# Kernel optimization log

Measured on AMD Instinct MI355X. Metric: run time of the kernel, lower is better.

Reference implementation:

```python
import jax, jax.numpy as jnp
import numpy as np

B, T, C, H = 4, 2048, 1024, 16
D = C // H  # head dim = 64


def setup_inputs() -> dict:
    key = jax.random.key(0)
    ks = jax.random.split(key, 8)
    s = 1.0 / np.sqrt(C)
    return {
        "x": jax.random.normal(ks[0], (B, T, C), jnp.float32),
        "mask": jax.random.randint(ks[1], (B, T), 0, 2, jnp.int32),
        "Wq": jax.random.normal(ks[2], (C, C), jnp.float32) * s,
        "bq": jnp.zeros((C,), jnp.float32),
        "Wk": jax.random.normal(ks[3], (C, C), jnp.float32) * s,
        "bk": jnp.zeros((C,), jnp.float32),
        "Wv": jax.random.normal(ks[4], (C, C), jnp.float32) * s,
        "bv": jnp.zeros((C,), jnp.float32),
    }


def reference(x, mask, Wq, bq, Wk, bk, Wv, bv):
    # QKV projections (nn.Linear: x @ W.T + b); W stored here as [out,in] -> use W.T
    q = x @ Wq.T + bq
    k = x @ Wk.T + bk
    v = x @ Wv.T + bv
    # split heads: [B,T,C] -> [B,H,T,D]
    q = q.reshape(B, T, H, D).transpose(0, 2, 1, 3)
    k = k.reshape(B, T, H, D).transpose(0, 2, 1, 3)
    v = v.reshape(B, T, H, D).transpose(0, 2, 1, 3)
    # scaled dot-product attention scores [B,H,T,T]
    attn = jnp.einsum("bhqd,bhkd->bhqk", q, k) / jnp.sqrt(jnp.float32(D))
    # additive mask over key positions: attn - inf*(1-mask), expressed stably
    big_neg = jnp.float32(-1e30)
    attn = jnp.where(mask[:, None, None, :] > 0, attn, big_neg)
    attn = jax.nn.softmax(attn, axis=-1)
    # dropout p=0 -> identity
    y = jnp.einsum("bhqk,bhkd->bhqd", attn, v)
    # merge heads: [B,H,T,D] -> [B,T,C]
    return y.transpose(0, 2, 1, 3).reshape(B, T, C)
```

## Files before the change

kernel.cpp:

```cpp
#include <hip/hip_runtime.h>
#include <stdint.h>

#define BB 4
#define TT 2048
#define CC 1024
#define HH 16
#define DD 64
#define MM (BB * TT)

typedef unsigned short u16;
typedef unsigned int   u32;
typedef __attribute__((ext_vector_type(8))) short short8;
typedef _Float16 half8  __attribute__((ext_vector_type(8)));
typedef __fp16   fp16x2 __attribute__((ext_vector_type(2)));
typedef __attribute__((ext_vector_type(4))) float f32x4;
typedef __attribute__((ext_vector_type(4))) unsigned short u16x4;
typedef __attribute__((ext_vector_type(4))) unsigned int u32x4;

#if __has_builtin(__builtin_amdgcn_exp2f)
#define EXP2(x) __builtin_amdgcn_exp2f(x)
#else
#define EXP2(x) __expf(0.69314718055994531f * (x))
#endif

__device__ inline u16 f2bf(float f) {
    union { float f; unsigned u; } v; v.f = f;
    unsigned r = 0x7fffu + ((v.u >> 16) & 1u);
    return (u16)((v.u + r) >> 16);
}
__device__ inline u16 f2h(float f) {
    union { _Float16 h; u16 u; } c; c.h = (_Float16)f; return c.u;
}
__device__ inline u32 pkh(float a, float b) {
    union { fp16x2 h; u32 u; } c;
    c.h = __builtin_amdgcn_cvt_pkrtz(a, b);
    return c.u;
}
__device__ inline u32 pkmask(int a, int b) {
    return ((u32)(-a) & 0xFFFFu) | ((u32)(-b) << 16);
}

#define NX (MM * CC / 4)
#define NW (CC * CC / 4)
__global__ void cvt_all(const float* __restrict__ x,  const float* __restrict__ Wq,
                        const float* __restrict__ Wk, const float* __restrict__ Wv,
                        u16* __restrict__ xb, u16* __restrict__ Wb) {
    int i = blockIdx.x * blockDim.x + threadIdx.x;
    const float* src; u16* dst; int j;
    if (i < NX)               { src = x;  dst = xb;                       j = i; }
    else if (i < NX + NW)     { src = Wq; dst = Wb;                       j = i - NX; }
    else if (i < NX + 2 * NW) { src = Wk; dst = Wb + (size_t)CC * CC;     j = i - NX - NW; }
    else if (i < NX + 3 * NW) { src = Wv; dst = Wb + (size_t)2 * CC * CC; j = i - NX - 2 * NW; }
    else return;
    float4 v = ((const float4*)src)[j];
    u16x4 o;
    o.x = f2bf(v.x); o.y = f2bf(v.y); o.z = f2bf(v.z); o.w = f2bf(v.w);
    ((u16x4*)dst)[j] = o;
}

__global__ void qkv_gemm(const u16* __restrict__ xb, const u16* __restrict__ Wb,
                         const float* __restrict__ bq, const float* __restrict__ bk,
                         const float* __restrict__ bv,
                         u16* __restrict__ Qh, u16* __restrict__ Kh, u16* __restrict__ Vt)
{
    const int z = blockIdx.z;
    const u16* W = Wb + (size_t)z * CC * CC;
    const float* bias = (z == 0) ? bq : ((z == 1) ? bk : bv);
    const float scale = (z == 0) ? 0.18033688011112042f : 1.0f;

    __shared__ __align__(16) u16 As[128][32];
    __shared__ __align__(16) u16 Bs[128][32];

    const int tid = threadIdx.x;
    const int l  = tid & 63, w = tid >> 6;
    const int wm = w >> 1,  wn = w & 1;
    const int lr = l & 15,  lq = l >> 4;
    const int m0 = blockIdx.y * 128, n0 = blockIdx.x * 128;

    f32x4 acc[4][4] = {};

    const u16* aLDS = (z == 2) ? &As[0][0] : &Bs[0][0];
    const u16* bLDS = (z == 2) ? &Bs[0][0] : &As[0][0];

    for (int kt = 0; kt < CC; kt += 32) {
        __syncthreads();
        #pragma unroll
        for (int r = 0; r < 2; ++r) {
            int c   = (r * 4 + w) * 64 + l;
            int row = c >> 2, kc = c & 3;
            const u16* ga = xb + (size_t)(m0 + row) * CC + kt + kc * 8;
            __builtin_amdgcn_global_load_lds(
                (const __attribute__((address_space(1))) void*)ga,
                (__attribute__((address_space(3))) void*)(&As[0][0] + (size_t)c * 8), 16, 0, 0);
            const u16* gb = W + (size_t)(n0 + row) * CC + kt + kc * 8;
            __builtin_amdgcn_global_load_lds(
                (const __attribute__((address_space(1))) void*)gb,
                (__attribute__((address_space(3))) void*)(&Bs[0][0] + (size_t)c * 8), 16, 0, 0);
        }
        __syncthreads();

        short8 af[4], bfr[4];
        #pragma unroll
        for (int mi = 0; mi < 4; ++mi)
            af[mi] = *(const short8*)(aLDS + (size_t)(wm * 64 + mi * 16 + lr) * 32 + lq * 8);
        #pragma unroll
        for (int ni = 0; ni < 4; ++ni)
            bfr[ni] = *(const short8*)(bLDS + (size_t)(wn * 64 + ni * 16 + lr) * 32 + lq * 8);
        #pragma unroll
        for (int mi = 0; mi < 4; ++mi)
            #pragma unroll
            for (int ni = 0; ni < 4; ++ni)
                acc[mi][ni] = __builtin_amdgcn_mfma_f32_16x16x32_bf16(
                    af[mi], bfr[ni], acc[mi][ni], 0, 0, 0);
    }

    if (z == 2) {
        #pragma unroll
        for (int ni = 0; ni < 4; ++ni) {
            int n = n0 + wn * 64 + ni * 16 + lr;
            float bvv = bias[n];
            int h = n >> 6, d = n & 63;
            #pragma unroll
            for (int mi = 0; mi < 4; ++mi) {
                int mbase = m0 + wm * 64 + mi * 16 + lq * 4;
                int b = mbase >> 11, t0 = mbase & (TT - 1);
                u16x4 pkv;
                #pragma unroll
                for (int r = 0; r < 4; ++r)
                    pkv[r] = f2h(acc[mi][ni][r] + bvv);
                *(u16x4*)&Vt[((size_t)(b * HH + h) * DD + d) * TT + t0] = pkv;
            }
        }
    } else {
        u16* out = (z == 0) ? Qh : Kh;
        #pragma unroll
        for (int mi = 0; mi < 4; ++mi) {
            int nb = n0 + wm * 64 + mi * 16 + lq * 4;
            float4 b4 = *(const float4*)&bias[nb];
            int h = nb >> 6, d0 = nb & 63;
            #pragma unroll
            for (int ni = 0; ni < 4; ++ni) {
                int m = m0 + wn * 64 + ni * 16 + lr;
                int b = m >> 11, t = m & (TT - 1);
                u16x4 pkv;
                pkv.x = f2h((acc[mi][ni][0] + b4.x) * scale);
                pkv.y = f2h((acc[mi][ni][1] + b4.y) * scale);
                pkv.z = f2h((acc[mi][ni][2] + b4.z) * scale);
                pkv.w = f2h((acc[mi][ni][3] + b4.w) * scale);
                *(u16x4*)&out[((size_t)(b * HH + h) * TT + t) * DD + d0] = pkv;
            }
        }
    }
}

__global__ __launch_bounds__(256, 4)
void attn_kernel(const u16* __restrict__ Qh, const u16* __restrict__ Kh,
                 const u16* __restrict__ Vt, const int* __restrict__ mask,
                 float* __restrict__ out)
{
    const int f   = blockIdx.x + (TT / 128) * (blockIdx.y + HH * blockIdx.z);
    const int xcd = f & 7, g = f >> 3;
    const int bh  = xcd * 8 + (g >> 4);
    const int qt  = g & 15;
    const int b   = bh >> 4, h = bh & 15;

    const int tid = threadIdx.x;
    const int l  = tid & 63, w = tid >> 6;
    const int lr = l & 15,  lq = l >> 4;

    __shared__ __align__(16) u16 Ks[2][64][72];
    __shared__ __align__(16) u16 Vs[2][2][64][40];

    const size_t base = (size_t)(b * HH + h) * TT * DD;
    const int q0 = qt * 128 + w * 32;

    half8 qf[2][2];
    #pragma unroll
    for (int qg = 0; qg < 2; ++qg)
        #pragma unroll
        for (int c = 0; c < 2; ++c)
            qf[qg][c] = *(const half8*)(Qh + base + (size_t)(q0 + qg * 16 + lr) * DD
                                        + c * 32 + lq * 8);

    const int kk = tid >> 3, dc = tid & 7;
    u16* k_dst0 = &Ks[0][kk][dc * 8];
    const u16* k_base = Kh + base + (size_t)kk * DD + dc * 8;
    const int vd = tid >> 2, vck = tid & 3;
    const int s0c = ((2 * vck) & 3) * 8 + (vck >> 1) * 4;
    const int s1c = ((2 * vck + 1) & 3) * 8 + (vck >> 1) * 4;
    u16* v_dst0a = &Vs[0][0][vd][s0c];
    u16* v_dst0b = &Vs[0][0][vd][s1c];
    const u16* v_base = Vt + base + (size_t)vd * TT + vck * 8;
    const int* mbase_p = mask + b * TT + 4 * lq;

    const int VHALF = 64 * 40;
    const int VBUF  = 2 * VHALF;
    const int KHALF = 32 * 72;
    const int KBUF  = 64 * 72;

    union { u32 u[4]; half8 h; } one_u;
    one_u.u[0] = one_u.u[1] = one_u.u[2] = one_u.u[3] = 0x3C003C00u;
    const half8 ones = one_u.h;

    {
        half8 k0 = *(const half8*)k_base;
        half8 k1 = *(const half8*)(k_base + 32 * DD);
        half8 v0 = *(const half8*)v_base;
        half8 v1 = *(const half8*)(v_base + 32);
        *(half8*)k_dst0 = k0;
        *(half8*)(k_dst0 + KHALF) = k1;
        #pragma unroll
        for (int hf = 0; hf < 2; ++hf) {
            half8 vv = hf ? v1 : v0;
            u16x4 va = { (u16)((u32x4&)vv)[0], (u16)(((u32x4&)vv)[0] >> 16),
                         (u16)((u32x4&)vv)[1], (u16)(((u32x4&)vv)[1] >> 16) };
            u16x4 vb = { (u16)((u32x4&)vv)[2], (u16)(((u32x4&)vv)[2] >> 16),
                         (u16)((u32x4&)vv)[3], (u16)(((u32x4&)vv)[3] >> 16) };
            *(u16x4*)(v_dst0a + hf * VHALF) = va;
            *(u16x4*)(v_dst0b + hf * VHALF) = vb;
        }
    }

    f32x4 o[2][5] = {};

    const int NT = TT / 64;
    __syncthreads();

    for (int kt = 0; kt < NT; ++kt) {
        const int p = kt & 1;
        int ktn = (kt + 1 < NT) ? kt + 1 : NT - 1;
        const u16* kp = k_base + (size_t)ktn * 64 * DD;
        half8 kreg0 = *(const half8*)kp;
        half8 kreg1 = *(const half8*)(kp + 32 * DD);
        const u16* vp = v_base + ktn * 64;
        half8 vreg0 = *(const half8*)vp;
        half8 vreg1 = *(const half8*)(vp + 32);
        int4 m0 = *(const int4*)(mbase_p + kt * 64);
        int4 m1 = *(const int4*)(mbase_p + kt * 64 + 16);
        int4 m2 = *(const int4*)(mbase_p + kt * 64 + 32);
        int4 m3 = *(const int4*)(mbase_p + kt * 64 + 48);

        half8 kf[4][2];
        #pragma unroll
        for (int kg = 0; kg < 4; ++kg)
            #pragma unroll
            for (int c = 0; c < 2; ++c)
                kf[kg][c] = *(const half8*)&Ks[p][kg * 16 + lr][c * 32 + lq * 8];

        f32x4 s[4][2];
        #pragma unroll
        for (int kg = 0; kg < 4; ++kg)
            #pragma unroll
            for (int qg = 0; qg < 2; ++qg) {
                f32x4 zz = {};
                zz = __builtin_amdgcn_mfma_f32_16x16x32_f16(kf[kg][0], qf[qg][0], zz, 0, 0, 0);
                zz = __builtin_amdgcn_mfma_f32_16x16x32_f16(kf[kg][1], qf[qg][1], zz, 0, 0, 0);
                s[kg][qg] = zz;
            }

        u32 am[8];
        am[0] = pkmask(m0.x, m0.y); am[1] = pkmask(m0.z, m0.w);
        am[2] = pkmask(m1.x, m1.y); am[3] = pkmask(m1.z, m1.w);
        am[4] = pkmask(m2.x, m2.y); am[5] = pkmask(m2.z, m2.w);
        am[6] = pkmask(m3.x, m3.y); am[7] = pkmask(m3.z, m3.w);

        half8 pf[2][2];
        #pragma unroll
        for (int hf = 0; hf < 2; ++hf)
            #pragma unroll
            for (int qg = 0; qg < 2; ++qg) {
                u32x4 pk;
                pk[0] = pkh(EXP2(s[2*hf][qg][0]),   EXP2(s[2*hf][qg][1]))   & am[4*hf];
                pk[1] = pkh(EXP2(s[2*hf][qg][2]),   EXP2(s[2*hf][qg][3]))   & am[4*hf+1];
                pk[2] = pkh(EXP2(s[2*hf+1][qg][0]), EXP2(s[2*hf+1][qg][1])) & am[4*hf+2];
                pk[3] = pkh(EXP2(s[2*hf+1][qg][2]), EXP2(s[2*hf+1][qg][3])) & am[4*hf+3];
                pf[hf][qg] = (half8&)pk;
            }

        #pragma unroll
        for (int hf = 0; hf < 2; ++hf) {
            #pragma unroll
            for (int dg = 0; dg < 4; ++dg) {
                half8 vf = *(const half8*)&Vs[p][hf][dg * 16 + lr][lq * 8];
                #pragma unroll
                for (int qg = 0; qg < 2; ++qg)
                    o[qg][dg] = __builtin_amdgcn_mfma_f32_16x16x32_f16(pf[hf][qg], vf, o[qg][dg], 0, 0, 0);
            }
            #pragma unroll
            for (int qg = 0; qg < 2; ++qg)
                o[qg][4] = __builtin_amdgcn_mfma_f32_16x16x32_f16(pf[hf][qg], ones, o[qg][4], 0, 0, 0);
        }

        u16* kd = k_dst0 + (p ^ 1) * KBUF;
        *(half8*)kd = kreg0;
        *(half8*)(kd + KHALF) = kreg1;
        #pragma unroll
        for (int hf = 0; hf < 2; ++hf) {
            half8 vv = hf ? vreg1 : vreg0;
            u16x4 va = { (u16)((u32x4&)vv)[0], (u16)(((u32x4&)vv)[0] >> 16),
                         (u16)((u32x4&)vv)[1], (u16)(((u32x4&)vv)[1] >> 16) };
            u16x4 vb = { (u16)((u32x4&)vv)[2], (u16)(((u32x4&)vv)[2] >> 16),
                         (u16)((u32x4&)vv)[3], (u16)(((u32x4&)vv)[3] >> 16) };
            *(u16x4*)(v_dst0a + (p ^ 1) * VBUF + hf * VHALF) = va;
            *(u16x4*)(v_dst0b + (p ^ 1) * VBUF + hf * VHALF) = vb;
        }
        __syncthreads();
    }

    #pragma unroll
    for (int qg = 0; qg < 2; ++qg)
        #pragma unroll
        for (int r = 0; r < 4; ++r) {
            float inv = 1.f / o[qg][4][r];
            int t = q0 + qg * 16 + lq * 4 + r;
            float* op = out + (size_t)(b * TT + t) * CC + h * DD;
            #pragma unroll
            for (int dg = 0; dg < 4; ++dg)
                op[dg * 16 + lr] = o[qg][dg][r] * inv;
        }
}

extern "C" void kernel_launch(void* const* d_in, const int* in_sizes, int n_in,
                              void* d_out, int out_size, void* d_ws, size_t ws_size,
                              hipStream_t stream) {
    const float* x    = (const float*)d_in[0];
    const int*   mask = (const int*)d_in[1];
    const float* Wq   = (const float*)d_in[2];
    const float* bq   = (const float*)d_in[3];
    const float* Wk   = (const float*)d_in[4];
    const float* bk   = (const float*)d_in[5];
    const float* Wv   = (const float*)d_in[6];
    const float* bv   = (const float*)d_in[7];
    float* out = (float*)d_out;

    u16* xb = (u16*)d_ws;
    u16* Wb = xb + (size_t)MM * CC;
    u16* Qh = Wb + (size_t)3 * CC * CC;
    u16* Kh = Qh + (size_t)MM * CC;
    u16* Vt = Kh + (size_t)MM * CC;

    {
        int total = NX + 3 * NW;
        cvt_all<<<(total + 255) / 256, 256, 0, stream>>>(x, Wq, Wk, Wv, xb, Wb);
    }

    qkv_gemm<<<dim3(CC / 128, MM / 128, 3), 256, 0, stream>>>(xb, Wb, bq, bk, bv, Qh, Kh, Vt);

    attn_kernel<<<dim3(TT / 128, HH, BB), 256, 0, stream>>>(Qh, Kh, Vt, mask, out);
}
```

Before: 257.7 us.

## Precompute packed mask, pre-permute V layout, and peel attention loop with priority hints

The mask is pre-packed into fp16 select words in the conversion kernel, so the attention loop loads two u32x4 per tile instead of four int4s and no longer builds the masks itself. The V-transposed output of the QKV GEMM is written in a permuted key order, which lets the attention kernel copy V into shared memory with plain 16-byte stores instead of unpacking and scattering. The main loop is peeled so the last iteration skips the redundant prefetch, mask loads are double-buffered in registers, and s_setprio is raised around the MFMA blocks. The cost is extra workspace and a more tightly coupled layout contract between the two kernels.

```diff
diff --git a/kernel.cpp b/kernel.cpp
--- a/kernel.cpp
+++ b/kernel.cpp
@@ -42,16 +42,28 @@
 
 #define NX (MM * CC / 4)
 #define NW (CC * CC / 4)
+#define NPM (BB * 1024)
 __global__ void cvt_all(const float* __restrict__ x,  const float* __restrict__ Wq,
                         const float* __restrict__ Wk, const float* __restrict__ Wv,
-                        u16* __restrict__ xb, u16* __restrict__ Wb) {
+                        const int* __restrict__ mask,
+                        u16* __restrict__ xb, u16* __restrict__ Wb,
+                        u32* __restrict__ pm) {
     int i = blockIdx.x * blockDim.x + threadIdx.x;
+    if (i >= NX + 3 * NW) {
+        int idx = i - (NX + 3 * NW);
+        if (idx < NPM) {
+            int b = idx >> 10, r = idx & 1023;
+            int kt = r >> 5, lq = (r >> 3) & 3, j = r & 7;
+            int key = kt * 64 + (j >> 2) * 32 + ((j >> 1) & 1) * 16 + lq * 4 + (j & 1) * 2;
+            pm[idx] = pkmask(mask[b * TT + key], mask[b * TT + key + 1]);
+        }
+        return;
+    }
     const float* src; u16* dst; int j;
     if (i < NX)               { src = x;  dst = xb;                       j = i; }
     else if (i < NX + NW)     { src = Wq; dst = Wb;                       j = i - NX; }
     else if (i < NX + 2 * NW) { src = Wk; dst = Wb + (size_t)CC * CC;     j = i - NX - NW; }
-    else if (i < NX + 3 * NW) { src = Wv; dst = Wb + (size_t)2 * CC * CC; j = i - NX - 2 * NW; }
-    else return;
+    else                      { src = Wv; dst = Wb + (size_t)2 * CC * CC; j = i - NX - 2 * NW; }
     float4 v = ((const float4*)src)[j];
     u16x4 o;
     o.x = f2bf(v.x); o.y = f2bf(v.y); o.z = f2bf(v.z); o.w = f2bf(v.w);
@@ -124,11 +136,13 @@
             for (int mi = 0; mi < 4; ++mi) {
                 int mbase = m0 + wm * 64 + mi * 16 + lq * 4;
                 int b = mbase >> 11, t0 = mbase & (TT - 1);
+                int gk  = (t0 >> 2) & 7;
+                int t0p = (t0 & ~31) | (((gk & 3) << 3) | ((gk >> 2) << 2));
                 u16x4 pkv;
                 #pragma unroll
                 for (int r = 0; r < 4; ++r)
                     pkv[r] = f2h(acc[mi][ni][r] + bvv);
-                *(u16x4*)&Vt[((size_t)(b * HH + h) * DD + d) * TT + t0] = pkv;
+                *(u16x4*)&Vt[((size_t)(b * HH + h) * DD + d) * TT + t0p] = pkv;
             }
         }
     } else {
@@ -155,7 +169,7 @@
 
 __global__ __launch_bounds__(256, 4)
 void attn_kernel(const u16* __restrict__ Qh, const u16* __restrict__ Kh,
-                 const u16* __restrict__ Vt, const int* __restrict__ mask,
+                 const u16* __restrict__ Vt, const u32* __restrict__ pm,
                  float* __restrict__ out)
 {
     const int f   = blockIdx.x + (TT / 128) * (blockIdx.y + HH * blockIdx.z);
@@ -186,12 +200,9 @@
     u16* k_dst0 = &Ks[0][kk][dc * 8];
     const u16* k_base = Kh + base + (size_t)kk * DD + dc * 8;
     const int vd = tid >> 2, vck = tid & 3;
-    const int s0c = ((2 * vck) & 3) * 8 + (vck >> 1) * 4;
-    const int s1c = ((2 * vck + 1) & 3) * 8 + (vck >> 1) * 4;
-    u16* v_dst0a = &Vs[0][0][vd][s0c];
-    u16* v_dst0b = &Vs[0][0][vd][s1c];
+    u16* v_dst0 = &Vs[0][0][vd][vck * 8];
     const u16* v_base = Vt + base + (size_t)vd * TT + vck * 8;
-    const int* mbase_p = mask + b * TT + 4 * lq;
+    const u32* pm_base = pm + b * 1024 + lq * 8;
 
     const int VHALF = 64 * 40;
     const int VBUF  = 2 * VHALF;
@@ -209,37 +220,19 @@
         half8 v1 = *(const half8*)(v_base + 32);
         *(half8*)k_dst0 = k0;
         *(half8*)(k_dst0 + KHALF) = k1;
-        #pragma unroll
-        for (int hf = 0; hf < 2; ++hf) {
-            half8 vv = hf ? v1 : v0;
-            u16x4 va = { (u16)((u32x4&)vv)[0], (u16)(((u32x4&)vv)[0] >> 16),
-                         (u16)((u32x4&)vv)[1], (u16)(((u32x4&)vv)[1] >> 16) };
-            u16x4 vb = { (u16)((u32x4&)vv)[2], (u16)(((u32x4&)vv)[2] >> 16),
-                         (u16)((u32x4&)vv)[3], (u16)(((u32x4&)vv)[3] >> 16) };
-            *(u16x4*)(v_dst0a + hf * VHALF) = va;
-            *(u16x4*)(v_dst0b + hf * VHALF) = vb;
-        }
+        *(half8*)v_dst0 = v0;
+        *(half8*)(v_dst0 + VHALF) = v1;
     }
 
     f32x4 o[2][5] = {};
+
+    u32x4 amc0 = *(const u32x4*)(pm_base);
+    u32x4 amc1 = *(const u32x4*)(pm_base + 4);
 
     const int NT = TT / 64;
     __syncthreads();
 
-    for (int kt = 0; kt < NT; ++kt) {
-        const int p = kt & 1;
-        int ktn = (kt + 1 < NT) ? kt + 1 : NT - 1;
-        const u16* kp = k_base + (size_t)ktn * 64 * DD;
-        half8 kreg0 = *(const half8*)kp;
-        half8 kreg1 = *(const half8*)(kp + 32 * DD);
-        const u16* vp = v_base + ktn * 64;
-        half8 vreg0 = *(const half8*)vp;
-        half8 vreg1 = *(const half8*)(vp + 32);
-        int4 m0 = *(const int4*)(mbase_p + kt * 64);
-        int4 m1 = *(const int4*)(mbase_p + kt * 64 + 16);
-        int4 m2 = *(const int4*)(mbase_p + kt * 64 + 32);
-        int4 m3 = *(const int4*)(mbase_p + kt * 64 + 48);
-
+    auto compute = [&](int p, u32x4 am0, u32x4 am1) {
         half8 kf[4][2];
         #pragma unroll
         for (int kg = 0; kg < 4; ++kg)
@@ -248,6 +241,7 @@
                 kf[kg][c] = *(const half8*)&Ks[p][kg * 16 + lr][c * 32 + lq * 8];
 
         f32x4 s[4][2];
+        __builtin_amdgcn_s_setprio(1);
         #pragma unroll
         for (int kg = 0; kg < 4; ++kg)
             #pragma unroll
@@ -257,26 +251,24 @@
                 zz = __builtin_amdgcn_mfma_f32_16x16x32_f16(kf[kg][1], qf[qg][1], zz, 0, 0, 0);
                 s[kg][qg] = zz;
             }
-
-        u32 am[8];
-        am[0] = pkmask(m0.x, m0.y); am[1] = pkmask(m0.z, m0.w);
-        am[2] = pkmask(m1.x, m1.y); am[3] = pkmask(m1.z, m1.w);
-        am[4] = pkmask(m2.x, m2.y); am[5] = pkmask(m2.z, m2.w);
-        am[6] = pkmask(m3.x, m3.y); am[7] = pkmask(m3.z, m3.w);
+        __builtin_amdgcn_s_setprio(0);
 
         half8 pf[2][2];
         #pragma unroll
-        for (int hf = 0; hf < 2; ++hf)
+        for (int hf = 0; hf < 2; ++hf) {
+            const u32x4 am = hf ? am1 : am0;
             #pragma unroll
             for (int qg = 0; qg < 2; ++qg) {
                 u32x4 pk;
-                pk[0] = pkh(EXP2(s[2*hf][qg][0]),   EXP2(s[2*hf][qg][1]))   & am[4*hf];
-                pk[1] = pkh(EXP2(s[2*hf][qg][2]),   EXP2(s[2*hf][qg][3]))   & am[4*hf+1];
-                pk[2] = pkh(EXP2(s[2*hf+1][qg][0]), EXP2(s[2*hf+1][qg][1])) & am[4*hf+2];
-                pk[3] = pkh(EXP2(s[2*hf+1][qg][2]), EXP2(s[2*hf+1][qg][3])) & am[4*hf+3];
+                pk[0] = pkh(EXP2(s[2*hf][qg][0]),   EXP2(s[2*hf][qg][1]))   & am[0];
+                pk[1] = pkh(EXP2(s[2*hf][qg][2]),   EXP2(s[2*hf][qg][3]))   & am[1];
+                pk[2] = pkh(EXP2(s[2*hf+1][qg][0]), EXP2(s[2*hf+1][qg][1])) & am[2];
+                pk[3] = pkh(EXP2(s[2*hf+1][qg][2]), EXP2(s[2*hf+1][qg][3])) & am[3];
                 pf[hf][qg] = (half8&)pk;
             }
-
+        }
+
+        __builtin_amdgcn_s_setprio(1);
         #pragma unroll
         for (int hf = 0; hf < 2; ++hf) {
             #pragma unroll
@@ -290,22 +282,32 @@
             for (int qg = 0; qg < 2; ++qg)
                 o[qg][4] = __builtin_amdgcn_mfma_f32_16x16x32_f16(pf[hf][qg], ones, o[qg][4], 0, 0, 0);
         }
+        __builtin_amdgcn_s_setprio(0);
+    };
+
+    for (int kt = 0; kt < NT - 1; ++kt) {
+        const int p = kt & 1;
+        const u16* kp = k_base + (size_t)(kt + 1) * 64 * DD;
+        half8 kreg0 = *(const half8*)kp;
+        half8 kreg1 = *(const half8*)(kp + 32 * DD);
+        const u16* vp = v_base + (kt + 1) * 64;
+        half8 vreg0 = *(const half8*)vp;
+        half8 vreg1 = *(const half8*)(vp + 32);
+        u32x4 amn0 = *(const u32x4*)(pm_base + (kt + 1) * 32);
+        u32x4 amn1 = *(const u32x4*)(pm_base + (kt + 1) * 32 + 4);
+
+        compute(p, amc0, amc1);
 
         u16* kd = k_dst0 + (p ^ 1) * KBUF;
         *(half8*)kd = kreg0;
         *(half8*)(kd + KHALF) = kreg1;
-        #pragma unroll
-        for (int hf = 0; hf < 2; ++hf) {
-            half8 vv = hf ? vreg1 : vreg0;
-            u16x4 va = { (u16)((u32x4&)vv)[0], (u16)(((u32x4&)vv)[0] >> 16),
-                         (u16)((u32x4&)vv)[1], (u16)(((u32x4&)vv)[1] >> 16) };
-            u16x4 vb = { (u16)((u32x4&)vv)[2], (u16)(((u32x4&)vv)[2] >> 16),
-                         (u16)((u32x4&)vv)[3], (u16)(((u32x4&)vv)[3] >> 16) };
-            *(u16x4*)(v_dst0a + (p ^ 1) * VBUF + hf * VHALF) = va;
-            *(u16x4*)(v_dst0b + (p ^ 1) * VBUF + hf * VHALF) = vb;
-        }
+        u16* vdst = v_dst0 + (p ^ 1) * VBUF;
+        *(half8*)vdst = vreg0;
+        *(half8*)(vdst + VHALF) = vreg1;
+        amc0 = amn0; amc1 = amn1;
         __syncthreads();
     }
+    compute((NT - 1) & 1, amc0, amc1);
 
     #pragma unroll
     for (int qg = 0; qg < 2; ++qg)
@@ -338,13 +340,14 @@
     u16* Qh = Wb + (size_t)3 * CC * CC;
     u16* Kh = Qh + (size_t)MM * CC;
     u16* Vt = Kh + (size_t)MM * CC;
+    u32* pm = (u32*)(Vt + (size_t)MM * CC);
 
     {
-        int total = NX + 3 * NW;
-        cvt_all<<<(total + 255) / 256, 256, 0, stream>>>(x, Wq, Wk, Wv, xb, Wb);
+        int total = NX + 3 * NW + NPM;
+        cvt_all<<<(total + 255) / 256, 256, 0, stream>>>(x, Wq, Wk, Wv, mask, xb, Wb, pm);
     }
 
     qkv_gemm<<<dim3(CC / 128, MM / 128, 3), 256, 0, stream>>>(xb, Wb, bq, bk, bv, Qh, Kh, Vt);
 
-    attn_kernel<<<dim3(TT / 128, HH, BB), 256, 0, stream>>>(Qh, Kh, Vt, mask, out);
-}
+    attn_kernel<<<dim3(TT / 128, HH, BB), 256, 0, stream>>>(Qh, Kh, Vt, pm, out);
+}
```

After: 319.0 us. +23.8%, slower.
